# Performance work log

Hardware: AMD Instinct MI355X
Metric: run time of the kernel (lower is better)

The kernel has to match this reference:

```python
import jax, jax.numpy as jnp
import numpy as np

DIM = 384
HEADS = 6
POINTS = 4
LEVELS = 3
FFN_DIM = 1024
EPS = 1e-6
SHAPES = [(128, 128), (64, 64), (32, 32)]  # (H, W) per level
B = 4
NQ = 4096


def layer_norm(x, g, b):
    m = jnp.mean(x, axis=-1, keepdims=True)
    v = jnp.mean(jnp.square(x - m), axis=-1, keepdims=True)
    return (x - m) * jax.lax.rsqrt(v + EPS) * g + b


def _bilinear_sample(vl, loc, h, w):
    # vl: [B, heads, Dh, h*w] per-level value; loc: [B, Nq, heads, P, 2] in [0,1]
    # grid_sample(align_corners=False, padding_mode='zeros') semantics
    Bn, Hh, Dh, _ = vl.shape
    Nq, P = loc.shape[1], loc.shape[3]
    x = loc[..., 0] * w - 0.5
    y = loc[..., 1] * h - 0.5
    x0 = jnp.floor(x); y0 = jnp.floor(y)
    wx1 = x - x0; wx0 = 1.0 - wx1
    wy1 = y - y0; wy0 = 1.0 - wy1
    acc = jnp.zeros((Bn, Hh, Dh, Nq, P), dtype=vl.dtype)
    for xi, yi, wgt in ((x0, y0, wx0 * wy0), (x0 + 1, y0, wx1 * wy0),
                        (x0, y0 + 1, wx0 * wy1), (x0 + 1, y0 + 1, wx1 * wy1)):
        valid = (xi >= 0) & (xi <= w - 1) & (yi >= 0) & (yi <= h - 1)
        idx = (jnp.clip(yi, 0, h - 1) * w + jnp.clip(xi, 0, w - 1)).astype(jnp.int32)
        idx = idx.transpose(0, 2, 1, 3).reshape(Bn, Hh, 1, Nq * P)  # [B,heads,1,Nq*P]
        g = jnp.take_along_axis(vl, jnp.broadcast_to(idx, (Bn, Hh, Dh, Nq * P)), axis=3)
        g = g.reshape(Bn, Hh, Dh, Nq, P)
        wm = (wgt * valid.astype(wgt.dtype)).transpose(0, 2, 1, 3)[:, :, None]  # [B,heads,1,Nq,P]
        acc = acc + g * wm
    return acc  # [B, heads, Dh, Nq, P]


def msda(query, value, reference_points, shapes_np, W_off, b_off, W_aw, b_aw, W_v, b_v, W_o, b_o):
    Bn, Nq, D = query.shape
    L = len(shapes_np)
    Dh = D // HEADS
    v = value @ W_v.T + b_v  # [B, Nv, D]
    offsets = (query @ W_off.T + b_off).reshape(Bn, Nq, HEADS, L, POINTS, 2)
    aw = (query @ W_aw.T + b_aw).reshape(Bn, Nq, HEADS, L * POINTS)
    aw = jax.nn.softmax(aw, axis=-1).reshape(Bn, Nq, HEADS, L, POINTS)
    # offset normalizer is [W, H] per level
    norm = jnp.asarray([[w, h] for (h, w) in shapes_np], dtype=query.dtype)
    loc = reference_points[:, :, None, :, None, :] + offsets / norm[None, None, None, :, None, :]
    out = jnp.zeros((Bn, Nq, HEADS, Dh), dtype=query.dtype)
    start = 0
    for l, (h, w) in enumerate(shapes_np):
        vl = v[:, start:start + h * w].reshape(Bn, h * w, HEADS, Dh)
        vl = vl.transpose(0, 2, 3, 1)  # [B, heads, Dh, h*w]
        sampled = _bilinear_sample(vl, loc[:, :, :, l], h, w)  # [B,heads,Dh,Nq,P]
        out = out + jnp.einsum('bhdqp,bqhp->bqhd', sampled, aw[:, :, :, l])
        start += h * w
    return out.reshape(Bn, Nq, D) @ W_o.T + b_o


def setup_inputs():
    key = jax.random.key(0)
    ks = jax.random.split(key, 16)
    nv = sum(h * w for h, w in SHAPES)
    s = 0.02
    f32 = jnp.float32
    return dict(
        query=jax.random.normal(ks[0], (B, NQ, DIM), f32),
        reference_points=jax.random.uniform(ks[1], (B, NQ, LEVELS, 2), f32),
        feat=jax.random.normal(ks[2], (B, nv, DIM), f32),
        spatial_shapes=jnp.asarray(SHAPES, jnp.int32),
        level_start_index=jnp.asarray(np.cumsum([0] + [h * w for h, w in SHAPES])[:-1], jnp.int32),
        qn_g=jnp.ones((DIM,), f32), qn_b=jnp.zeros((DIM,), f32),
        fn_g=jnp.ones((DIM,), f32), fn_b=jnp.zeros((DIM,), f32),
        W_off=jax.random.normal(ks[3], (HEADS * LEVELS * POINTS * 2, DIM), f32) * s,
        b_off=jax.random.normal(ks[4], (HEADS * LEVELS * POINTS * 2,), f32) * s,
        W_aw=jax.random.normal(ks[5], (HEADS * LEVELS * POINTS, DIM), f32) * s,
        b_aw=jnp.zeros((HEADS * LEVELS * POINTS,), f32),
        W_v=jax.random.normal(ks[6], (DIM, DIM), f32) * s, b_v=jnp.zeros((DIM,), f32),
        W_o=jax.random.normal(ks[7], (DIM, DIM), f32) * s, b_o=jnp.zeros((DIM,), f32),
        n1_g=jnp.ones((DIM,), f32), n1_b=jnp.zeros((DIM,), f32),
        W1=jax.random.normal(ks[8], (FFN_DIM, DIM), f32) * s, b1=jnp.zeros((FFN_DIM,), f32),
        W2=jax.random.normal(ks[9], (DIM, FFN_DIM), f32) * s, b2=jnp.zeros((DIM,), f32),
        n2_g=jnp.ones((DIM,), f32), n2_b=jnp.zeros((DIM,), f32),
        gamma=jnp.full((DIM,), 0.01, f32),
    )


def reference(query, reference_points, feat, spatial_shapes, level_start_index,
              qn_g, qn_b, fn_g, fn_b,
              W_off, b_off, W_aw, b_aw, W_v, b_v, W_o, b_o,
              n1_g, n1_b, W1, b1, W2, b2, n2_g, n2_b, gamma):
    shapes_np = [tuple(int(v) for v in row) for row in np.asarray(spatial_shapes)]
    qn = layer_norm(query, qn_g, qn_b)
    fn = layer_norm(feat, fn_g, fn_b)
    # cross_attn (mmcv MSDeformAttn adds identity=query internally, dropout=0)
    x = qn + msda(qn, fn, reference_points, shapes_np,
                  W_off, b_off, W_aw, b_aw, W_v, b_v, W_o, b_o)
    x = layer_norm(x, n1_g, n1_b)
    x = x + (jax.nn.gelu(x @ W1.T + b1) @ W2.T + b2)  # FFN with residual
    x = layer_norm(x, n2_g, n2_b)
    return query + gamma * x
```

## Files before the change

### kernel.cpp

```cpp
#include <hip/hip_runtime.h>
#include <hip/hip_bf16.h>

#define DIMD 384
#define HEADS 6
#define DH 64
#define LEVELS 3
#define POINTS 4
#define FFN 1024
#define BB 4
#define NQ 4096
#define NV 21504
#define MQ (BB*NQ)
#define MV (BB*NV)
#define EPSF 1e-6f

typedef __hip_bfloat16 bf16;
typedef __attribute__((ext_vector_type(8))) short bf16x8;
typedef __attribute__((ext_vector_type(4))) float f32x4;

__device__ __forceinline__ float wave_sum(float v){
  #pragma unroll
  for(int o=32;o;o>>=1) v += __shfl_xor(v,o);
  return v;
}

#define NPREP 4609
__global__ __launch_bounds__(256) void pre_k(
  const float* __restrict__ Wv, const float* __restrict__ Wo,
  const float* __restrict__ W1, const float* __restrict__ W2,
  const float* __restrict__ Woff, const float* __restrict__ Waw,
  const float* __restrict__ boff, const float* __restrict__ baw,
  bf16* __restrict__ wv, bf16* __restrict__ wo, bf16* __restrict__ w1,
  bf16* __restrict__ w2, bf16* __restrict__ wcat, float* __restrict__ bcat,
  const float* __restrict__ feat, const float* __restrict__ fg,
  const float* __restrict__ fb, bf16* __restrict__ featn,
  const float* __restrict__ query, const float* __restrict__ qg,
  const float* __restrict__ qb, bf16* __restrict__ qn)
{
  const int blk = blockIdx.x;
  if(blk < NPREP){
    int i = blk*256 + threadIdx.x;
    if(i < 147456){ wv[i] = __float2bfloat16(Wv[i]); return; }
    i -= 147456;
    if(i < 147456){ wo[i] = __float2bfloat16(Wo[i]); return; }
    i -= 147456;
    if(i < 393216){ w1[i] = __float2bfloat16(W1[i]); return; }
    i -= 393216;
    if(i < 393216){ w2[i] = __float2bfloat16(W2[i]); return; }
    i -= 393216;
    if(i < 98304){
      int r = i/384, c = i - r*384;
      float v = r<144 ? Woff[r*384+c] : (r<216 ? Waw[(r-144)*384+c] : 0.f);
      wcat[i] = __float2bfloat16(v); return;
    }
    i -= 98304;
    if(i < 256){ bcat[i] = i<144 ? boff[i] : (i<216 ? baw[i-144] : 0.f); }
    return;
  }
  const int lblk = blk - NPREP;
  const float *x, *g, *b; bf16* o; int row0;
  if(lblk < MV/16){ x=feat;  g=fg; b=fb; o=featn; row0 = lblk*16; }
  else            { x=query; g=qg; b=qb; o=qn;    row0 = (lblk - MV/16)*16; }
  const int row = row0 + (threadIdx.x>>4);
  const int li  = threadIdx.x & 15;
  float4 va[6];
  float s=0.f, s2=0.f;
  const float* xr = x + (size_t)row*DIMD + li*4;
  #pragma unroll
  for(int j=0;j<6;j++){
    va[j] = *(const float4*)(xr + j*64);
    s  += va[j].x + va[j].y + va[j].z + va[j].w;
    s2 += va[j].x*va[j].x + va[j].y*va[j].y + va[j].z*va[j].z + va[j].w*va[j].w;
  }
  #pragma unroll
  for(int off=1; off<16; off<<=1){ s += __shfl_xor(s,off); s2 += __shfl_xor(s2,off); }
  const float m = s*(1.f/DIMD);
  const float r = rsqrtf(s2*(1.f/DIMD) - m*m + EPSF);
  #pragma unroll
  for(int j=0;j<6;j++){
    const int col = li*4 + j*64;
    const float4 g4 = *(const float4*)(g + col);
    const float4 b4 = *(const float4*)(b + col);
    short4 o4;
    o4.x = __builtin_bit_cast(short, __float2bfloat16((va[j].x-m)*r*g4.x + b4.x));
    o4.y = __builtin_bit_cast(short, __float2bfloat16((va[j].y-m)*r*g4.y + b4.y));
    o4.z = __builtin_bit_cast(short, __float2bfloat16((va[j].z-m)*r*g4.z + b4.z));
    o4.w = __builtin_bit_cast(short, __float2bfloat16((va[j].w-m)*r*g4.w + b4.w));
    *(short4*)((short*)o + (size_t)row*DIMD + col) = o4;
  }
}

#define NVB (MV/64)
__global__ __launch_bounds__(512,2) void gemm2_k(
    const bf16* __restrict__ A1, const bf16* __restrict__ B1,
    const float* __restrict__ bias1, bf16* __restrict__ out1,
    const bf16* __restrict__ A2, const bf16* __restrict__ B2,
    const float* __restrict__ bias2, float* __restrict__ out2)
{
  __shared__ __align__(16) short As[64*64];
  __shared__ __align__(16) short Bs[384*64];
  const int tid = threadIdx.x;
  const int wid = tid>>6, lane = tid&63;
  const int lr8 = lane>>3, lc8 = (lane&7)*8;
  const int cg = lane>>4;
  const bool vbr = blockIdx.x < NVB;

  if(vbr){
    const int m0 = blockIdx.x*64;
    f32x4 acc[4][3] = {};
    for(int k0=0; k0<DIMD; k0+=64){
      {
        const bf16* srcA = A1 + (size_t)(m0 + wid*8 + lr8)*DIMD + k0 + lc8;
        __builtin_amdgcn_global_load_lds((const __attribute__((address_space(1))) void*)srcA,
            (__attribute__((address_space(3))) void*)(As + wid*512), 16, 0, 0);
      }
      #pragma unroll
      for(int u=0;u<6;u++){
        const int t = wid*6 + u;
        const bf16* srcB = B1 + (size_t)(t*8 + lr8)*DIMD + k0 + lc8;
        __builtin_amdgcn_global_load_lds((const __attribute__((address_space(1))) void*)srcB,
            (__attribute__((address_space(3))) void*)(Bs + t*512), 16, 0, 0);
      }
      asm volatile("s_waitcnt vmcnt(0)" ::: "memory");
      __syncthreads();
      #pragma unroll
      for(int ks=0;ks<2;ks++){
        const int cbase = ks*32 + cg*8;
        bf16x8 af[4], bfr[3];
        #pragma unroll
        for(int i=0;i<4;i++)
          af[i] = *(const bf16x8*)(As + (i*16 + (lane&15))*64 + cbase);
        #pragma unroll
        for(int j=0;j<3;j++)
          bfr[j] = *(const bf16x8*)(Bs + (wid*48 + j*16 + (lane&15))*64 + cbase);
        #pragma unroll
        for(int i=0;i<4;i++)
          #pragma unroll
          for(int j=0;j<3;j++)
            acc[i][j] = __builtin_amdgcn_mfma_f32_16x16x32_bf16(af[i], bfr[j], acc[i][j], 0,0,0);
      }
      __syncthreads();
    }
    #pragma unroll
    for(int i=0;i<4;i++){
      const int r0 = m0 + i*16 + cg*4;
      #pragma unroll
      for(int j=0;j<3;j++){
        const int col = wid*48 + j*16 + (lane&15);
        const float bv = bias1[col];
        #pragma unroll
        for(int rr=0;rr<4;rr++)
          out1[(size_t)(r0+rr)*DIMD + col] = __float2bfloat16(acc[i][j][rr] + bv);
      }
    }
  } else {
    const int m0 = (blockIdx.x - NVB)*64;
    f32x4 acc[4][2] = {};
    for(int k0=0; k0<DIMD; k0+=64){
      {
        const bf16* srcA = A2 + (size_t)(m0 + wid*8 + lr8)*DIMD + k0 + lc8;
        __builtin_amdgcn_global_load_lds((const __attribute__((address_space(1))) void*)srcA,
            (__attribute__((address_space(3))) void*)(As + wid*512), 16, 0, 0);
      }
      #pragma unroll
      for(int u=0;u<4;u++){
        const int t = wid*4 + u;
        const bf16* srcB = B2 + (size_t)(t*8 + lr8)*DIMD + k0 + lc8;
        __builtin_amdgcn_global_load_lds((const __attribute__((address_space(1))) void*)srcB,
            (__attribute__((address_space(3))) void*)(Bs + t*512), 16, 0, 0);
      }
      asm volatile("s_waitcnt vmcnt(0)" ::: "memory");
      __syncthreads();
      #pragma unroll
      for(int ks=0;ks<2;ks++){
        const int cbase = ks*32 + cg*8;
        bf16x8 af[4], bfr[2];
        #pragma unroll
        for(int i=0;i<4;i++)
          af[i] = *(const bf16x8*)(As + (i*16 + (lane&15))*64 + cbase);
        #pragma unroll
        for(int j=0;j<2;j++)
          bfr[j] = *(const bf16x8*)(Bs + (wid*32 + j*16 + (lane&15))*64 + cbase);
        #pragma unroll
        for(int i=0;i<4;i++)
          #pragma unroll
          for(int j=0;j<2;j++)
            acc[i][j] = __builtin_amdgcn_mfma_f32_16x16x32_bf16(af[i], bfr[j], acc[i][j], 0,0,0);
      }
      __syncthreads();
    }
    #pragma unroll
    for(int i=0;i<4;i++){
      const int r0 = m0 + i*16 + cg*4;
      #pragma unroll
      for(int j=0;j<2;j++){
        const int col = wid*32 + j*16 + (lane&15);
        if(col >= 216) continue;
        const float bv = bias2[col];
        #pragma unroll
        for(int rr=0;rr<4;rr++)
          out2[(size_t)(r0+rr)*216 + col] = acc[i][j][rr] + bv;
      }
    }
  }
}

template<int KK,int MODE,int TM>
__global__ __launch_bounds__(512,2) void gl_k(
    const bf16* __restrict__ A, const bf16* __restrict__ Bw,
    const float* __restrict__ bias, const bf16* __restrict__ res,
    const float* __restrict__ g, const float* __restrict__ b,
    const float* __restrict__ gam, const float* __restrict__ qsrc,
    void* __restrict__ out)
{
  constexpr int MI = TM/16;
  __shared__ __align__(16) short As[64*64];
  __shared__ __align__(16) short Bs[384*64];
  __shared__ float wst[8*64*2];
  __shared__ float st[64*2];
  const int tid = threadIdx.x;
  const int wid = tid>>6, lane = tid&63;
  const int m0 = blockIdx.x*TM;
  const int lr8 = lane>>3, lc8 = (lane&7)*8;
  const int cg = lane>>4;
  f32x4 acc[MI][3] = {};

  for(int k0=0; k0<KK; k0+=64){
    if(wid < TM/8){
      const bf16* srcA = A + (size_t)(m0 + wid*8 + lr8)*KK + k0 + lc8;
      __builtin_amdgcn_global_load_lds((const __attribute__((address_space(1))) void*)srcA,
          (__attribute__((address_space(3))) void*)(As + wid*512), 16, 0, 0);
    }
    #pragma unroll
    for(int u=0;u<6;u++){
      const int t = wid*6 + u;
      const bf16* srcB = Bw + (size_t)(t*8 + lr8)*KK + k0 + lc8;
      __builtin_amdgcn_global_load_lds((const __attribute__((address_space(1))) void*)srcB,
          (__attribute__((address_space(3))) void*)(Bs + t*512), 16, 0, 0);
    }
    asm volatile("s_waitcnt vmcnt(0)" ::: "memory");
    __syncthreads();
    #pragma unroll
    for(int ks=0;ks<2;ks++){
      const int cbase = ks*32 + cg*8;
      bf16x8 af[MI], bfr[3];
      #pragma unroll
      for(int i=0;i<MI;i++)
        af[i] = *(const bf16x8*)(As + (i*16 + (lane&15))*64 + cbase);
      #pragma unroll
      for(int j=0;j<3;j++)
        bfr[j] = *(const bf16x8*)(Bs + (wid*48 + j*16 + (lane&15))*64 + cbase);
      #pragma unroll
      for(int i=0;i<MI;i++)
        #pragma unroll
        for(int j=0;j<3;j++)
          acc[i][j] = __builtin_amdgcn_mfma_f32_16x16x32_bf16(af[i], bfr[j], acc[i][j], 0,0,0);
    }
    __syncthreads();
  }

  float sA[MI][4], sB[MI][4];
  #pragma unroll
  for(int i=0;i<MI;i++)
    #pragma unroll
    for(int rr=0;rr<4;rr++){ sA[i][rr]=0.f; sB[i][rr]=0.f; }
  #pragma unroll
  for(int i=0;i<MI;i++){
    #pragma unroll
    for(int j=0;j<3;j++){
      const int col = wid*48 + j*16 + (lane&15);
      const float bv = bias[col];
      #pragma unroll
      for(int rr=0;rr<4;rr++){
        const int rowg = m0 + i*16 + cg*4 + rr;
        float v = acc[i][j][rr] + bv
                + __bfloat162float(res[(size_t)rowg*DIMD + col]);
        acc[i][j][rr] = v;
        sA[i][rr] += v; sB[i][rr] += v*v;
      }
    }
  }
  #pragma unroll
  for(int off=1; off<16; off<<=1){
    #pragma unroll
    for(int i=0;i<MI;i++)
      #pragma unroll
      for(int rr=0;rr<4;rr++){
        sA[i][rr] += __shfl_xor(sA[i][rr], off);
        sB[i][rr] += __shfl_xor(sB[i][rr], off);
      }
  }
  if((lane&15)==0){
    #pragma unroll
    for(int i=0;i<MI;i++)
      #pragma unroll
      for(int rr=0;rr<4;rr++){
        const int row = i*16 + cg*4 + rr;
        wst[(wid*TM + row)*2 + 0] = sA[i][rr];
        wst[(wid*TM + row)*2 + 1] = sB[i][rr];
      }
  }
  __syncthreads();
  if(tid < TM){
    float ms=0.f, m2=0.f;
    #pragma unroll
    for(int w=0;w<8;w++){ ms += wst[(w*TM+tid)*2]; m2 += wst[(w*TM+tid)*2+1]; }
    const float m  = ms*(1.f/DIMD);
    const float rs = rsqrtf(m2*(1.f/DIMD) - m*m + EPSF);
    st[tid*2] = m; st[tid*2+1] = rs;
  }
  __syncthreads();
  #pragma unroll
  for(int i=0;i<MI;i++){
    #pragma unroll
    for(int j=0;j<3;j++){
      const int col = wid*48 + j*16 + (lane&15);
      const float gc = g[col], bc = b[col];
      #pragma unroll
      for(int rr=0;rr<4;rr++){
        const int row = i*16 + cg*4 + rr;
        const int rowg = m0 + row;
        const float t = (acc[i][j][rr] - st[row*2])*st[row*2+1]*gc + bc;
        if constexpr(MODE == 1){
          ((bf16*)out)[(size_t)rowg*DIMD + col] = __float2bfloat16(t);
        } else {
          ((float*)out)[(size_t)rowg*DIMD + col] =
              qsrc[(size_t)rowg*DIMD + col] + gam[col]*t;
        }
      }
    }
  }
}

template<int GELU_,int STBF>
__global__ __launch_bounds__(256) void mgemm_k(
    const bf16* __restrict__ A, const bf16* __restrict__ Bw,
    const float* __restrict__ bias, void* __restrict__ Cv,
    int M, int K, int Nreal, int ldc)
{
  __shared__ __align__(16) short As[128*64];
  __shared__ __align__(16) short Bs[128*64];
  const int tid  = threadIdx.x;
  const int wid  = tid>>6, lane = tid&63;
  const int wr   = wid>>1, wc = wid&1;
  const int m0   = blockIdx.y*128, n0 = blockIdx.x*128;
  f32x4 acc[4][4] = {};

  const int sr = (lane>>3);
  const int sc = (lane&7)*8;

  for(int k0=0; k0<K; k0+=64){
    #pragma unroll
    for(int u=0;u<4;u++){
      const int t = wid*4 + u;
      const int r = t*8 + sr;
      const bf16* srcA = A  + (size_t)(m0+r)*K + k0 + sc;
      const bf16* srcB = Bw + (size_t)(n0+r)*K + k0 + sc;
      __builtin_amdgcn_global_load_lds((const __attribute__((address_space(1))) void*)srcA,
          (__attribute__((address_space(3))) void*)(As + t*512), 16, 0, 0);
      __builtin_amdgcn_global_load_lds((const __attribute__((address_space(1))) void*)srcB,
          (__attribute__((address_space(3))) void*)(Bs + t*512), 16, 0, 0);
    }
    asm volatile("s_waitcnt vmcnt(0)" ::: "memory");
    __syncthreads();
    #pragma unroll
    for(int ks=0;ks<2;ks++){
      bf16x8 af[4], bfr[4];
      #pragma unroll
      for(int i=0;i<4;i++){
        const int ar = wr*64 + i*16 + (lane&15);
        af[i]  = *(const bf16x8*)(As + ar*64 + ks*32 + (lane>>4)*8);
        const int br = wc*64 + i*16 + (lane&15);
        bfr[i] = *(const bf16x8*)(Bs + br*64 + ks*32 + (lane>>4)*8);
      }
      #pragma unroll
      for(int i=0;i<4;i++)
        #pragma unroll
        for(int j=0;j<4;j++)
          acc[i][j] = __builtin_amdgcn_mfma_f32_16x16x32_bf16(af[i], bfr[j], acc[i][j], 0,0,0);
    }
    __syncthreads();
  }
  #pragma unroll
  for(int i=0;i<4;i++){
    const int rbase = m0 + wr*64 + i*16 + (lane>>4)*4;
    #pragma unroll
    for(int j=0;j<4;j++){
      const int col = n0 + wc*64 + j*16 + (lane&15);
      if(col >= Nreal) continue;
      const float bv = bias[col];
      #pragma unroll
      for(int rr=0;rr<4;rr++){
        const int rowg = rbase + rr;
        float v = acc[i][j][rr] + bv;
        if constexpr(GELU_){ float u=v; v = 0.5f*u*(1.f+tanhf(0.7978845608028654f*(u+0.044715f*u*u*u))); }
        if constexpr(STBF) ((bf16*)Cv)[(size_t)rowg*ldc + col] = __float2bfloat16(v);
        else               ((float*)Cv)[(size_t)rowg*ldc + col] = v;
      }
    }
  }
}

__global__ __launch_bounds__(256) void msda_k(
    const bf16* __restrict__ v, const float* __restrict__ offaw,
    const float* __restrict__ refp, const int* __restrict__ sshapes,
    const int* __restrict__ lstart, bf16* __restrict__ out)
{
  __shared__ uint2 plds[8][48];
  const int bid = blockIdx.x;
  const int pid0 = ((bid & 7)*1536 + (bid >> 3))*8;
  const int tid = threadIdx.x;
  if(tid < 96){
    const int pl = tid/12, p12 = tid - pl*12;
    const int pid = pid0 + pl;
    const int bq = pid/6, h = pid - bq*6;
    const int b  = bq >> 12;
    const float* row = offaw + (size_t)bq*216;
    float mx = -1e30f;
    #pragma unroll
    for(int i=0;i<12;i++) mx = fmaxf(mx, row[144 + h*12 + i]);
    float ssum = 0.f, my = 0.f;
    #pragma unroll
    for(int i=0;i<12;i++){
      const float e = __expf(row[144 + h*12 + i] - mx);
      ssum += e;
      if(i==p12) my = e;
    }
    const float aww = my/ssum;
    const int l = p12>>2;
    const int hh = sshapes[2*l], ww = sshapes[2*l+1];
    const int st = lstart[l];
    const float rx = refp[((size_t)bq*LEVELS + l)*2 + 0];
    const float ry = refp[((size_t)bq*LEVELS + l)*2 + 1];
    const float ox = row[(h*12 + p12)*2 + 0];
    const float oy = row[(h*12 + p12)*2 + 1];
    const float px = (rx + ox/(float)ww)*(float)ww - 0.5f;
    const float py = (ry + oy/(float)hh)*(float)hh - 0.5f;
    const float fx0 = floorf(px), fy0 = floorf(py);
    const int x0 = (int)fx0, y0 = (int)fy0;
    const float wx1 = px - fx0, wx0 = 1.f - wx1;
    const float wy1 = py - fy0, wy0 = 1.f - wy1;
    #pragma unroll
    for(int c=0;c<4;c++){
      const int xi = x0 + (c&1);
      const int yi = y0 + (c>>1);
      const float wgt = (c&1 ? wx1 : wx0) * (c>>1 ? wy1 : wy0);
      const bool valid = (xi>=0) & (xi<=ww-1) & (yi>=0) & (yi<=hh-1);
      const int cx = min(max(xi,0), ww-1);
      const int cy = min(max(yi,0), hh-1);
      const unsigned off = (unsigned)((((b*NV + st + cy*ww + cx)*DIMD) + h*DH)*2);
      uint2 pr; pr.x = off; pr.y = __float_as_uint(valid ? wgt*aww : 0.f);
      plds[pl][p12*4 + c] = pr;
    }
  }
  __syncthreads();
  const int pl  = (tid>>5);
  const int pid = pid0 + pl;
  const int ch  = tid & 31;
  const char* vb = (const char*)v;
  float a0 = 0.f, a1 = 0.f;
  #pragma unroll
  for(int c=0;c<48;c++){
    const uint2 pr = plds[pl][c];
    const unsigned g = *(const unsigned*)(vb + pr.x + (ch<<2));
    const float w = __uint_as_float(pr.y);
    a0 = fmaf(w, __uint_as_float(g << 16), a0);
    a1 = fmaf(w, __uint_as_float(g & 0xffff0000u), a1);
  }
  const int bq = pid/6, h = pid - bq*6;
  const unsigned u0 = (unsigned)__builtin_bit_cast(unsigned short, __float2bfloat16(a0));
  const unsigned u1 = (unsigned)__builtin_bit_cast(unsigned short, __float2bfloat16(a1));
  *(unsigned*)((char*)out + (size_t)bq*768 + h*128 + (ch<<2)) = u0 | (u1<<16);
}

static inline size_t rnd(size_t x){ return (x + 511) & ~(size_t)511; }

extern "C" void kernel_launch(void* const* d_in, const int* in_sizes, int n_in,
                              void* d_out, int out_size, void* d_ws, size_t ws_size,
                              hipStream_t stream)
{
  const float* query = (const float*)d_in[0];
  const float* refp  = (const float*)d_in[1];
  const float* feat  = (const float*)d_in[2];
  const int*   sshp  = (const int*)d_in[3];
  const int*   lst   = (const int*)d_in[4];
  const float* qn_g  = (const float*)d_in[5];
  const float* qn_b  = (const float*)d_in[6];
  const float* fn_g  = (const float*)d_in[7];
  const float* fn_b  = (const float*)d_in[8];
  const float* W_off = (const float*)d_in[9];
  const float* b_off = (const float*)d_in[10];
  const float* W_aw  = (const float*)d_in[11];
  const float* b_aw  = (const float*)d_in[12];
  const float* W_v   = (const float*)d_in[13];
  const float* b_v   = (const float*)d_in[14];
  const float* W_o   = (const float*)d_in[15];
  const float* b_o   = (const float*)d_in[16];
  const float* n1_g  = (const float*)d_in[17];
  const float* n1_b  = (const float*)d_in[18];
  const float* W1    = (const float*)d_in[19];
  const float* b1    = (const float*)d_in[20];
  const float* W2    = (const float*)d_in[21];
  const float* b2    = (const float*)d_in[22];
  const float* n2_g  = (const float*)d_in[23];
  const float* n2_b  = (const float*)d_in[24];
  const float* gam   = (const float*)d_in[25];

  char* p = (char*)d_ws;
  bf16* featn = (bf16*)p;
  char* late  = p;
  p += rnd((size_t)MV*DIMD*2);
  bf16* vbuf  = (bf16*)p;  p += rnd((size_t)MV*DIMD*2);
  bf16* qn    = (bf16*)p;  p += rnd((size_t)MQ*DIMD*2);
  bf16* wv    = (bf16*)p;  p += rnd((size_t)147456*2);
  bf16* wo    = (bf16*)p;  p += rnd((size_t)147456*2);
  bf16* w1    = (bf16*)p;  p += rnd((size_t)393216*2);
  bf16* w2    = (bf16*)p;  p += rnd((size_t)393216*2);
  bf16* wcat  = (bf16*)p;  p += rnd((size_t)98304*2);
  float* bcat = (float*)p; p += rnd((size_t)256*4);
  bf16* hbuf  = (bf16*)p;  p += rnd((size_t)MQ*FFN*2);
  float* offaw = (float*)p; p += rnd((size_t)MQ*216*4);
  char* q2 = late;
  bf16*  msda  = (bf16*)q2;  q2 += rnd((size_t)MQ*DIMD*2);
  bf16*  x2    = (bf16*)q2;  q2 += rnd((size_t)MQ*DIMD*2);

  pre_k<<<NPREP + MV/16 + MQ/16, 256, 0, stream>>>(
      W_v, W_o, W1, W2, W_off, W_aw, b_off, b_aw,
      wv, wo, w1, w2, wcat, bcat,
      feat, fn_g, fn_b, featn, query, qn_g, qn_b, qn);
  gemm2_k<<<NVB + MQ/64, 512, 0, stream>>>(featn, wv, b_v, vbuf,
                                           qn, wcat, bcat, offaw);
  msda_k<<<MQ*HEADS/8, 256, 0, stream>>>(vbuf, offaw, refp, sshp, lst, msda);
  gl_k<DIMD,1,32><<<MQ/32, 512, 0, stream>>>(msda, wo, b_o, qn,
                                             n1_g, n1_b, nullptr, nullptr, x2);
  mgemm_k<1,1><<<dim3(8, MQ/128), 256, 0, stream>>>(x2, w1, b1, hbuf,
                                                    MQ, DIMD, FFN, FFN);
  gl_k<FFN,2,32><<<MQ/32, 512, 0, stream>>>(hbuf, w2, b2, x2,
                                            n2_g, n2_b, gam, query, (float*)d_out);
}
```

Measured before the change: 245.6 us.

## Fold feature LayerNorm into value projection GEMM epilogue

Removes the separate normalization pass over the feature tensor and its bf16 intermediate. The LN gain is folded into the W_v weights, and the GEMM now loads raw fp32 features into LDS, accumulating row sum and sum of squares alongside the MFMA loop. The epilogue applies rs*acc - m*rs*u1 + c0, where u1 and c0 are precomputed column reductions of W_v with gamma and beta. This saves a full read and write of the large feature tensor, at the cost of doubled LDS A-tile traffic, fp32-to-bf16 conversion in the inner loop, and slightly different numerics since the mean is subtracted after rounding.

```diff
diff --git a/kernel.cpp b/kernel.cpp
--- a/kernel.cpp
+++ b/kernel.cpp
@@ -24,23 +24,38 @@
   return v;
 }
 
+__device__ __forceinline__ bf16x8 cvt8(f32x4 a, f32x4 b){
+  bf16x8 r;
+  r[0]=__builtin_bit_cast(short,__float2bfloat16(a[0]));
+  r[1]=__builtin_bit_cast(short,__float2bfloat16(a[1]));
+  r[2]=__builtin_bit_cast(short,__float2bfloat16(a[2]));
+  r[3]=__builtin_bit_cast(short,__float2bfloat16(a[3]));
+  r[4]=__builtin_bit_cast(short,__float2bfloat16(b[0]));
+  r[5]=__builtin_bit_cast(short,__float2bfloat16(b[1]));
+  r[6]=__builtin_bit_cast(short,__float2bfloat16(b[2]));
+  r[7]=__builtin_bit_cast(short,__float2bfloat16(b[3]));
+  return r;
+}
+
 #define NPREP 4609
+#define NVPREP 96
 __global__ __launch_bounds__(256) void pre_k(
   const float* __restrict__ Wv, const float* __restrict__ Wo,
   const float* __restrict__ W1, const float* __restrict__ W2,
   const float* __restrict__ Woff, const float* __restrict__ Waw,
   const float* __restrict__ boff, const float* __restrict__ baw,
-  bf16* __restrict__ wv, bf16* __restrict__ wo, bf16* __restrict__ w1,
+  const float* __restrict__ fng, const float* __restrict__ fnb,
+  const float* __restrict__ bv,
+  bf16* __restrict__ wvg, bf16* __restrict__ wo, bf16* __restrict__ w1,
   bf16* __restrict__ w2, bf16* __restrict__ wcat, float* __restrict__ bcat,
-  const float* __restrict__ feat, const float* __restrict__ fg,
-  const float* __restrict__ fb, bf16* __restrict__ featn,
+  float* __restrict__ u1, float* __restrict__ c0,
   const float* __restrict__ query, const float* __restrict__ qg,
   const float* __restrict__ qb, bf16* __restrict__ qn)
 {
   const int blk = blockIdx.x;
   if(blk < NPREP){
     int i = blk*256 + threadIdx.x;
-    if(i < 147456){ wv[i] = __float2bfloat16(Wv[i]); return; }
+    if(i < 147456){ wvg[i] = __float2bfloat16(Wv[i] * fng[i % 384]); return; }
     i -= 147456;
     if(i < 147456){ wo[i] = __float2bfloat16(Wo[i]); return; }
     i -= 147456;
@@ -57,15 +72,26 @@
     if(i < 256){ bcat[i] = i<144 ? boff[i] : (i<216 ? baw[i-144] : 0.f); }
     return;
   }
-  const int lblk = blk - NPREP;
-  const float *x, *g, *b; bf16* o; int row0;
-  if(lblk < MV/16){ x=feat;  g=fg; b=fb; o=featn; row0 = lblk*16; }
-  else            { x=query; g=qg; b=qb; o=qn;    row0 = (lblk - MV/16)*16; }
-  const int row = row0 + (threadIdx.x>>4);
+  if(blk < NPREP + NVPREP){
+    const int n = (blk - NPREP)*4 + (threadIdx.x>>6);
+    const int lane = threadIdx.x & 63;
+    float s1=0.f, s0=0.f;
+    #pragma unroll
+    for(int i=0;i<6;i++){
+      const int k = lane + i*64;
+      const float w = Wv[(size_t)n*DIMD + k];
+      s1 += w*fng[k]; s0 += w*fnb[k];
+    }
+    s1 = wave_sum(s1); s0 = wave_sum(s0);
+    if(lane==0){ u1[n] = s1; c0[n] = s0 + bv[n]; }
+    return;
+  }
+  const int lblk = blk - NPREP - NVPREP;
+  const int row = lblk*16 + (threadIdx.x>>4);
   const int li  = threadIdx.x & 15;
   float4 va[6];
   float s=0.f, s2=0.f;
-  const float* xr = x + (size_t)row*DIMD + li*4;
+  const float* xr = query + (size_t)row*DIMD + li*4;
   #pragma unroll
   for(int j=0;j<6;j++){
     va[j] = *(const float4*)(xr + j*64);
@@ -79,26 +105,29 @@
   #pragma unroll
   for(int j=0;j<6;j++){
     const int col = li*4 + j*64;
-    const float4 g4 = *(const float4*)(g + col);
-    const float4 b4 = *(const float4*)(b + col);
+    const float4 g4 = *(const float4*)(qg + col);
+    const float4 b4 = *(const float4*)(qb + col);
     short4 o4;
     o4.x = __builtin_bit_cast(short, __float2bfloat16((va[j].x-m)*r*g4.x + b4.x));
     o4.y = __builtin_bit_cast(short, __float2bfloat16((va[j].y-m)*r*g4.y + b4.y));
     o4.z = __builtin_bit_cast(short, __float2bfloat16((va[j].z-m)*r*g4.z + b4.z));
     o4.w = __builtin_bit_cast(short, __float2bfloat16((va[j].w-m)*r*g4.w + b4.w));
-    *(short4*)((short*)o + (size_t)row*DIMD + col) = o4;
+    *(short4*)((short*)qn + (size_t)row*DIMD + col) = o4;
   }
 }
 
 #define NVB (MV/64)
 __global__ __launch_bounds__(512,2) void gemm2_k(
-    const bf16* __restrict__ A1, const bf16* __restrict__ B1,
-    const float* __restrict__ bias1, bf16* __restrict__ out1,
+    const float* __restrict__ feat, const bf16* __restrict__ wvg,
+    const float* __restrict__ u1, const float* __restrict__ c0,
+    bf16* __restrict__ out1,
     const bf16* __restrict__ A2, const bf16* __restrict__ B2,
     const float* __restrict__ bias2, float* __restrict__ out2)
 {
-  __shared__ __align__(16) short As[64*64];
+  __shared__ __align__(16) float AsF[64*64];
   __shared__ __align__(16) short Bs[384*64];
+  __shared__ float st[64*2];
+  short* As = (short*)AsF;
   const int tid = threadIdx.x;
   const int wid = tid>>6, lane = tid&63;
   const int lr8 = lane>>3, lc8 = (lane&7)*8;
@@ -107,29 +136,46 @@
 
   if(vbr){
     const int m0 = blockIdx.x*64;
+    const int srow = tid>>3, scol = (tid&7)*8;
     f32x4 acc[4][3] = {};
+    float s=0.f, s2=0.f;
     for(int k0=0; k0<DIMD; k0+=64){
-      {
-        const bf16* srcA = A1 + (size_t)(m0 + wid*8 + lr8)*DIMD + k0 + lc8;
+      #pragma unroll
+      for(int u=0;u<2;u++){
+        const int t = wid*2 + u;
+        const float* srcA = feat + (size_t)(m0 + t*4 + (lane>>4))*DIMD + k0 + (lane&15)*4;
         __builtin_amdgcn_global_load_lds((const __attribute__((address_space(1))) void*)srcA,
-            (__attribute__((address_space(3))) void*)(As + wid*512), 16, 0, 0);
+            (__attribute__((address_space(3))) void*)(AsF + t*256), 16, 0, 0);
       }
       #pragma unroll
       for(int u=0;u<6;u++){
         const int t = wid*6 + u;
-        const bf16* srcB = B1 + (size_t)(t*8 + lr8)*DIMD + k0 + lc8;
+        const bf16* srcB = wvg + (size_t)(t*8 + lr8)*DIMD + k0 + lc8;
         __builtin_amdgcn_global_load_lds((const __attribute__((address_space(1))) void*)srcB,
             (__attribute__((address_space(3))) void*)(Bs + t*512), 16, 0, 0);
       }
       asm volatile("s_waitcnt vmcnt(0)" ::: "memory");
       __syncthreads();
+      {
+        f32x4 p0 = *(const f32x4*)(AsF + srow*64 + scol);
+        f32x4 p1 = *(const f32x4*)(AsF + srow*64 + scol + 4);
+        #pragma unroll
+        for(int e=0;e<4;e++){
+          s += p0[e] + p1[e];
+          s2 += p0[e]*p0[e] + p1[e]*p1[e];
+        }
+      }
       #pragma unroll
       for(int ks=0;ks<2;ks++){
         const int cbase = ks*32 + cg*8;
         bf16x8 af[4], bfr[3];
         #pragma unroll
-        for(int i=0;i<4;i++)
-          af[i] = *(const bf16x8*)(As + (i*16 + (lane&15))*64 + cbase);
+        for(int i=0;i<4;i++){
+          const int ar = i*16 + (lane&15);
+          f32x4 q0 = *(const f32x4*)(AsF + ar*64 + cbase);
+          f32x4 q1 = *(const f32x4*)(AsF + ar*64 + cbase + 4);
+          af[i] = cvt8(q0, q1);
+        }
         #pragma unroll
         for(int j=0;j<3;j++)
           bfr[j] = *(const bf16x8*)(Bs + (wid*48 + j*16 + (lane&15))*64 + cbase);
@@ -141,16 +187,26 @@
       }
       __syncthreads();
     }
+    s  += __shfl_xor(s,1);  s  += __shfl_xor(s,2);  s  += __shfl_xor(s,4);
+    s2 += __shfl_xor(s2,1); s2 += __shfl_xor(s2,2); s2 += __shfl_xor(s2,4);
+    if((tid&7)==0){
+      const float m  = s*(1.f/DIMD);
+      const float rs = rsqrtf(s2*(1.f/DIMD) - m*m + EPSF);
+      st[2*srow] = rs; st[2*srow+1] = m*rs;
+    }
+    __syncthreads();
     #pragma unroll
     for(int i=0;i<4;i++){
-      const int r0 = m0 + i*16 + cg*4;
       #pragma unroll
       for(int j=0;j<3;j++){
         const int col = wid*48 + j*16 + (lane&15);
-        const float bv = bias1[col];
-        #pragma unroll
-        for(int rr=0;rr<4;rr++)
-          out1[(size_t)(r0+rr)*DIMD + col] = __float2bfloat16(acc[i][j][rr] + bv);
+        const float u1c = u1[col], c0c = c0[col];
+        #pragma unroll
+        for(int rr=0;rr<4;rr++){
+          const int r = i*16 + cg*4 + rr;
+          const float v = st[2*r]*acc[i][j][rr] - st[2*r+1]*u1c + c0c;
+          out1[(size_t)(m0+r)*DIMD + col] = __float2bfloat16(v);
+        }
       }
     }
   } else {
@@ -507,28 +563,27 @@
   const float* gam   = (const float*)d_in[25];
 
   char* p = (char*)d_ws;
-  bf16* featn = (bf16*)p;
-  char* late  = p;
-  p += rnd((size_t)MV*DIMD*2);
   bf16* vbuf  = (bf16*)p;  p += rnd((size_t)MV*DIMD*2);
   bf16* qn    = (bf16*)p;  p += rnd((size_t)MQ*DIMD*2);
-  bf16* wv    = (bf16*)p;  p += rnd((size_t)147456*2);
+  bf16* wvg   = (bf16*)p;  p += rnd((size_t)147456*2);
   bf16* wo    = (bf16*)p;  p += rnd((size_t)147456*2);
   bf16* w1    = (bf16*)p;  p += rnd((size_t)393216*2);
   bf16* w2    = (bf16*)p;  p += rnd((size_t)393216*2);
   bf16* wcat  = (bf16*)p;  p += rnd((size_t)98304*2);
   float* bcat = (float*)p; p += rnd((size_t)256*4);
+  float* u1   = (float*)p; p += rnd((size_t)384*4);
+  float* c0   = (float*)p; p += rnd((size_t)384*4);
   bf16* hbuf  = (bf16*)p;  p += rnd((size_t)MQ*FFN*2);
   float* offaw = (float*)p; p += rnd((size_t)MQ*216*4);
-  char* q2 = late;
-  bf16*  msda  = (bf16*)q2;  q2 += rnd((size_t)MQ*DIMD*2);
-  bf16*  x2    = (bf16*)q2;  q2 += rnd((size_t)MQ*DIMD*2);
-
-  pre_k<<<NPREP + MV/16 + MQ/16, 256, 0, stream>>>(
+  bf16*  msda  = (bf16*)p;  p += rnd((size_t)MQ*DIMD*2);
+  bf16*  x2    = (bf16*)p;  p += rnd((size_t)MQ*DIMD*2);
+
+  pre_k<<<NPREP + NVPREP + MQ/16, 256, 0, stream>>>(
       W_v, W_o, W1, W2, W_off, W_aw, b_off, b_aw,
-      wv, wo, w1, w2, wcat, bcat,
-      feat, fn_g, fn_b, featn, query, qn_g, qn_b, qn);
-  gemm2_k<<<NVB + MQ/64, 512, 0, stream>>>(featn, wv, b_v, vbuf,
+      fn_g, fn_b, b_v,
+      wvg, wo, w1, w2, wcat, bcat, u1, c0,
+      query, qn_g, qn_b, qn);
+  gemm2_k<<<NVB + MQ/64, 512, 0, stream>>>(feat, wvg, u1, c0, vbuf,
                                            qn, wcat, bcat, offaw);
   msda_k<<<MQ*HEADS/8, 256, 0, stream>>>(vbuf, offaw, refp, sshp, lst, msda);
   gl_k<DIMD,1,32><<<MQ/32, 512, 0, stream>>>(msda, wo, b_o, qn,
```

Result: slower. 269.4 us (+9.7%).
